# Kernel optimization log

Hardware: AMD Instinct MI355X
Metric: run time of the kernel (lower is better)

The kernel has to match this reference:

```python
import jax, jax.numpy as jnp
import numpy as np

LOWERSIZE = 40


def setup_inputs() -> dict:
    key = jax.random.key(0)
    ks = jax.random.split(key, 6)
    N, x_dim, y_dim = 2048, 768, 768
    return {
        "x_samples": jax.random.normal(ks[0], (N, x_dim), dtype=jnp.float32),
        "y_samples": jax.random.normal(ks[1], (N, y_dim), dtype=jnp.float32),
        "W1": jax.random.normal(ks[2], (LOWERSIZE, x_dim + y_dim), dtype=jnp.float32) * 0.02,
        "b1": jax.random.normal(ks[3], (LOWERSIZE,), dtype=jnp.float32) * 0.02,
        "W2": jax.random.normal(ks[4], (1, LOWERSIZE), dtype=jnp.float32) * 0.02,
        "b2": jax.random.normal(ks[5], (1,), dtype=jnp.float32) * 0.02,
    }


def reference(x_samples, y_samples, W1, b1, W2, b2):
    # F(z) = W2 @ relu(W1 @ z + b1) + b2, z = cat(x, y)
    N = y_samples.shape[0]
    x_dim = x_samples.shape[1]
    W1x = W1[:, :x_dim]   # [40, x_dim]
    W1y = W1[:, x_dim:]   # [40, y_dim]

    # Diagonal term T0: F(cat(x_i, y_i)) -> [N, 1]
    h0 = jax.nn.relu(x_samples @ W1x.T + y_samples @ W1y.T + b1)
    T0 = h0 @ W2.T + b2

    # Pairwise term: T1[i, j] = F(cat(x_j, y_i)) - 1.
    # Split the first Linear over x and y to avoid materializing the
    # [N, N, x_dim+y_dim] concatenation (same math, linearity of W1).
    hx = x_samples @ W1x.T  # [N, 40]
    hy = y_samples @ W1y.T  # [N, 40]
    h = jax.nn.relu(hy[:, None, :] + hx[None, :, :] + b1)  # [N, N, 40]
    T1 = (h @ W2.T + b2 - 1.0)[..., 0]  # [N, N]

    lse = jax.nn.logsumexp(T1, axis=1) - jnp.log(jnp.float32(N))  # [N]
    lower_bound = T0.mean() - jnp.exp(lse).mean()
    return lower_bound
```

## Files before the change

kernel.cpp:

```cpp
#include <hip/hip_runtime.h>

#define NROWS 2048
#define KDIM  768
#define L     40
#define KCH   6
#define KCSZ  128
#define HN    (NROWS * L)

__global__ __launch_bounds__(256) void k_proj(const float* __restrict__ x,
                                              const float* __restrict__ y,
                                              const float* __restrict__ W1,
                                              float* __restrict__ part) {
    const int kc    = blockIdx.y;
    const int which = blockIdx.z;
    const float* __restrict__ A = which ? y : x;
    const int tid = threadIdx.x;
    const int r   = tid >> 4;
    const int seg = tid & 15;
    const int row0 = blockIdx.x * 16;

    __shared__ float sh[16 * 688];

    const float* arow = A + (size_t)(row0 + r) * KDIM + kc * KCSZ;
    float4 a0 = *(const float4*)(arow + seg * 4);
    float4 a1 = *(const float4*)(arow + 64 + seg * 4);

    const float* wbase = W1 + (size_t)which * KDIM + kc * KCSZ;
#pragma unroll 8
    for (int o = 0; o < L; ++o) {
        const float* wrow = wbase + (size_t)o * (2 * KDIM);
        float4 w0 = *(const float4*)(wrow + seg * 4);
        float4 w1 = *(const float4*)(wrow + 64 + seg * 4);
        float s = a0.x * w0.x + a0.y * w0.y + a0.z * w0.z + a0.w * w0.w
                + a1.x * w1.x + a1.y * w1.y + a1.z * w1.z + a1.w * w1.w;
        sh[r * 688 + o * 17 + seg] = s;
    }
    __syncthreads();

    float* pout = part + (size_t)(kc * 2 + which) * HN + (size_t)row0 * L;
    for (int idx = tid; idx < 16 * L; idx += 256) {
        int rr = idx / L;
        int o  = idx - rr * L;
        float s = 0.f;
        int base = rr * 688 + o * 17;
#pragma unroll
        for (int q = 0; q < 16; ++q) s += sh[base + q];
        pout[idx] = s;
    }
}

__global__ __launch_bounds__(256) void k_red(const float* __restrict__ part,
                                             const float* __restrict__ b1,
                                             float* __restrict__ hxb,
                                             float* __restrict__ hy) {
    int gid = blockIdx.x * 256 + threadIdx.x;
    int which = gid / HN;
    int rem   = gid - which * HN;
    float s = 0.f;
#pragma unroll
    for (int kc = 0; kc < KCH; ++kc)
        s += part[(size_t)(kc * 2 + which) * HN + rem];
    if (!which) {
        s += b1[rem % L];
        hxb[rem] = s;
    } else {
        hy[rem] = s;
    }
}

#define BI 128
#define BJ 64
#define STRD 44

__global__ __launch_bounds__(512) void k_pair(const float* __restrict__ hxb,
                                              const float* __restrict__ hy,
                                              const float* __restrict__ W2,
                                              const float* __restrict__ b2p,
                                              float* __restrict__ pairE,
                                              float* __restrict__ pairT) {
    __shared__ float shy[BI * STRD];
    __shared__ float shx[BJ * STRD];
    __shared__ float sw2[STRD];
    __shared__ float red[16];

    const int tid = threadIdx.x;
    const int i0 = blockIdx.x * BI;
    const int j0 = blockIdx.y * BJ;

    for (int idx = tid; idx < BI * 10; idx += 512) {
        int rr = idx / 10, c = idx - rr * 10;
        float4 v = ((const float4*)(hy + (size_t)i0 * L))[idx];
        *(float4*)(shy + rr * STRD + c * 4) = v;
    }
    for (int idx = tid; idx < BJ * 10; idx += 512) {
        int rr = idx / 10, c = idx - rr * 10;
        float4 v = ((const float4*)(hxb + (size_t)j0 * L))[idx];
        *(float4*)(shx + rr * STRD + c * 4) = v;
    }
    if (tid < 10) ((float4*)sw2)[tid] = ((const float4*)W2)[tid];
    __syncthreads();

    const int tx = tid & 15, ty = tid >> 4;

    float acc[4][4];
#pragma unroll
    for (int u = 0; u < 4; ++u)
#pragma unroll
        for (int v = 0; v < 4; ++v) acc[u][v] = 0.f;

#pragma unroll
    for (int k4 = 0; k4 < 10; ++k4) {
        float4 w = *(const float4*)(sw2 + k4 * 4);
        float4 ay[4], ax[4];
#pragma unroll
        for (int u = 0; u < 4; ++u)
            ay[u] = *(const float4*)(shy + (ty + 32 * u) * STRD + k4 * 4);
#pragma unroll
        for (int v = 0; v < 4; ++v)
            ax[v] = *(const float4*)(shx + (tx + 16 * v) * STRD + k4 * 4);
#pragma unroll
        for (int u = 0; u < 4; ++u)
#pragma unroll
            for (int v = 0; v < 4; ++v) {
                float t;
                t = ay[u].x + ax[v].x; t = fmaxf(t, 0.f); acc[u][v] += t * w.x;
                t = ay[u].y + ax[v].y; t = fmaxf(t, 0.f); acc[u][v] += t * w.y;
                t = ay[u].z + ax[v].z; t = fmaxf(t, 0.f); acc[u][v] += t * w.z;
                t = ay[u].w + ax[v].w; t = fmaxf(t, 0.f); acc[u][v] += t * w.w;
            }
    }

    const float b2v = b2p[0];
    const float c1  = b2v - 1.f;
    float sumE = 0.f, sumT = 0.f;
#pragma unroll
    for (int u = 0; u < 4; ++u)
#pragma unroll
        for (int v = 0; v < 4; ++v) {
            int gi = i0 + ty + 32 * u;
            int gj = j0 + tx + 16 * v;
            float val = acc[u][v];
            if (gi == gj) sumT += val + b2v;
            sumE += __expf(val + c1);
        }

#pragma unroll
    for (int off = 32; off > 0; off >>= 1) {
        sumE += __shfl_down(sumE, off);
        sumT += __shfl_down(sumT, off);
    }
    int wid = tid >> 6;
    if ((tid & 63) == 0) { red[wid] = sumE; red[8 + wid] = sumT; }
    __syncthreads();
    if (tid == 0) {
        float e = 0.f, t = 0.f;
#pragma unroll
        for (int q = 0; q < 8; ++q) { e += red[q]; t += red[8 + q]; }
        int bid = blockIdx.y * gridDim.x + blockIdx.x;
        pairE[bid] = e;
        pairT[bid] = t;
    }
}

__global__ __launch_bounds__(512) void k_fin(const float* __restrict__ pairE,
                                             const float* __restrict__ pairT,
                                             float* __restrict__ out) {
    __shared__ float red[16];
    const int tid = threadIdx.x;
    float e = pairE[tid];
    float t = pairT[tid];
#pragma unroll
    for (int off = 32; off > 0; off >>= 1) {
        e += __shfl_down(e, off);
        t += __shfl_down(t, off);
    }
    int wid = tid >> 6;
    if ((tid & 63) == 0) { red[wid] = e; red[8 + wid] = t; }
    __syncthreads();
    if (tid == 0) {
        float se = 0.f, st = 0.f;
#pragma unroll
        for (int q = 0; q < 8; ++q) { se += red[q]; st += red[8 + q]; }
        const float invN = 1.0f / (float)NROWS;
        out[0] = st * invN - se * invN * invN;
    }
}

extern "C" void kernel_launch(void* const* d_in, const int* in_sizes, int n_in,
                              void* d_out, int out_size, void* d_ws, size_t ws_size,
                              hipStream_t stream) {
    const float* x  = (const float*)d_in[0];
    const float* y  = (const float*)d_in[1];
    const float* W1 = (const float*)d_in[2];
    const float* b1 = (const float*)d_in[3];
    const float* W2 = (const float*)d_in[4];
    const float* b2 = (const float*)d_in[5];
    float* out = (float*)d_out;

    float* wsf   = (float*)d_ws;
    float* hxb   = wsf;
    float* hy    = hxb + HN;
    float* part  = hy + HN;
    float* pairE = part + (size_t)KCH * 2 * HN;
    float* pairT = pairE + 512;

    k_proj<<<dim3(NROWS / 16, KCH, 2), 256, 0, stream>>>(x, y, W1, part);
    k_red<<<(2 * HN) / 256, 256, 0, stream>>>(part, b1, hxb, hy);
    k_pair<<<dim3(NROWS / BI, NROWS / BJ), 512, 0, stream>>>(hxb, hy, W2, b2, pairE, pairT);
    k_fin<<<1, 512, 0, stream>>>(pairE, pairT, out);
}
```

Before: 99.99 us.

## Process two rows per thread in projection and double-buffer pair kernel LDS loads

The projection kernel now has each thread handle two rows, so each W1 load is reused twice. It pre-reduces the partial sums with a cross-lane shuffle, which halves shared-memory stores and the final reduction work, and the grid shrinks accordingly. The pair kernel manually double-buffers its LDS operand loads across k4 steps and adds a min-blocks-per-CU launch bound so loads can overlap the ReLU/FMA work. The double buffering raises register pressure and could hurt occupancy despite the hint.

```diff
diff --git a/kernel.cpp b/kernel.cpp
--- a/kernel.cpp
+++ b/kernel.cpp
@@ -6,6 +6,8 @@
 #define KCH   6
 #define KCSZ  128
 #define HN    (NROWS * L)
+
+#define PSTR 328
 
 __global__ __launch_bounds__(256) void k_proj(const float* __restrict__ x,
                                               const float* __restrict__ y,
@@ -17,13 +19,16 @@
     const int tid = threadIdx.x;
     const int r   = tid >> 4;
     const int seg = tid & 15;
-    const int row0 = blockIdx.x * 16;
-
-    __shared__ float sh[16 * 688];
-
-    const float* arow = A + (size_t)(row0 + r) * KDIM + kc * KCSZ;
-    float4 a0 = *(const float4*)(arow + seg * 4);
-    float4 a1 = *(const float4*)(arow + 64 + seg * 4);
+    const int row0 = blockIdx.x * 32;
+
+    __shared__ float sh[32 * PSTR];
+
+    const float* arowA = A + (size_t)(row0 + r) * KDIM + kc * KCSZ;
+    const float* arowB = A + (size_t)(row0 + 16 + r) * KDIM + kc * KCSZ;
+    float4 a0 = *(const float4*)(arowA + seg * 4);
+    float4 a1 = *(const float4*)(arowA + 64 + seg * 4);
+    float4 b0 = *(const float4*)(arowB + seg * 4);
+    float4 b1 = *(const float4*)(arowB + 64 + seg * 4);
 
     const float* wbase = W1 + (size_t)which * KDIM + kc * KCSZ;
 #pragma unroll 8
@@ -31,21 +36,28 @@
         const float* wrow = wbase + (size_t)o * (2 * KDIM);
         float4 w0 = *(const float4*)(wrow + seg * 4);
         float4 w1 = *(const float4*)(wrow + 64 + seg * 4);
-        float s = a0.x * w0.x + a0.y * w0.y + a0.z * w0.z + a0.w * w0.w
-                + a1.x * w1.x + a1.y * w1.y + a1.z * w1.z + a1.w * w1.w;
-        sh[r * 688 + o * 17 + seg] = s;
+        float sA = a0.x * w0.x + a0.y * w0.y + a0.z * w0.z + a0.w * w0.w
+                 + a1.x * w1.x + a1.y * w1.y + a1.z * w1.z + a1.w * w1.w;
+        float sB = b0.x * w0.x + b0.y * w0.y + b0.z * w0.z + b0.w * w0.w
+                 + b1.x * w1.x + b1.y * w1.y + b1.z * w1.z + b1.w * w1.w;
+        sA += __shfl_xor(sA, 8);
+        sB += __shfl_xor(sB, 8);
+        if (seg < 8) {
+            sh[r * PSTR + o * 8 + seg] = sA;
+            sh[(r + 16) * PSTR + o * 8 + seg] = sB;
+        }
     }
     __syncthreads();
 
     float* pout = part + (size_t)(kc * 2 + which) * HN + (size_t)row0 * L;
-    for (int idx = tid; idx < 16 * L; idx += 256) {
+#pragma unroll
+    for (int k = 0; k < 5; ++k) {
+        int idx = tid + k * 256;
         int rr = idx / L;
         int o  = idx - rr * L;
-        float s = 0.f;
-        int base = rr * 688 + o * 17;
-#pragma unroll
-        for (int q = 0; q < 16; ++q) s += sh[base + q];
-        pout[idx] = s;
+        const float4* p = (const float4*)(sh + rr * PSTR + o * 8);
+        float4 u0 = p[0], u1 = p[1];
+        pout[idx] = u0.x + u0.y + u0.z + u0.w + u1.x + u1.y + u1.z + u1.w;
     }
 }
 
@@ -72,12 +84,12 @@
 #define BJ 64
 #define STRD 44
 
-__global__ __launch_bounds__(512) void k_pair(const float* __restrict__ hxb,
-                                              const float* __restrict__ hy,
-                                              const float* __restrict__ W2,
-                                              const float* __restrict__ b2p,
-                                              float* __restrict__ pairE,
-                                              float* __restrict__ pairT) {
+__global__ __launch_bounds__(512, 4) void k_pair(const float* __restrict__ hxb,
+                                                 const float* __restrict__ hy,
+                                                 const float* __restrict__ W2,
+                                                 const float* __restrict__ b2p,
+                                                 float* __restrict__ pairE,
+                                                 float* __restrict__ pairT) {
     __shared__ float shy[BI * STRD];
     __shared__ float shx[BJ * STRD];
     __shared__ float sw2[STRD];
@@ -108,27 +120,43 @@
 #pragma unroll
         for (int v = 0; v < 4; ++v) acc[u][v] = 0.f;
 
-#pragma unroll
-    for (int k4 = 0; k4 < 10; ++k4) {
-        float4 w = *(const float4*)(sw2 + k4 * 4);
-        float4 ay[4], ax[4];
-#pragma unroll
-        for (int u = 0; u < 4; ++u)
-            ay[u] = *(const float4*)(shy + (ty + 32 * u) * STRD + k4 * 4);
-#pragma unroll
-        for (int v = 0; v < 4; ++v)
-            ax[v] = *(const float4*)(shx + (tx + 16 * v) * STRD + k4 * 4);
-#pragma unroll
-        for (int u = 0; u < 4; ++u)
-#pragma unroll
-            for (int v = 0; v < 4; ++v) {
-                float t;
-                t = ay[u].x + ax[v].x; t = fmaxf(t, 0.f); acc[u][v] += t * w.x;
-                t = ay[u].y + ax[v].y; t = fmaxf(t, 0.f); acc[u][v] += t * w.y;
-                t = ay[u].z + ax[v].z; t = fmaxf(t, 0.f); acc[u][v] += t * w.z;
-                t = ay[u].w + ax[v].w; t = fmaxf(t, 0.f); acc[u][v] += t * w.w;
-            }
-    }
+    float4 ayA[4], axA[4], wA4;
+    float4 ayB[4], axB[4], wB4;
+
+#define LOADF(AY, AX, W4, K4) do {                                          \
+    W4 = *(const float4*)(sw2 + (K4) * 4);                                  \
+    _Pragma("unroll") for (int u_ = 0; u_ < 4; ++u_)                        \
+        AY[u_] = *(const float4*)(shy + (ty + 32 * u_) * STRD + (K4) * 4);  \
+    _Pragma("unroll") for (int v_ = 0; v_ < 4; ++v_)                        \
+        AX[v_] = *(const float4*)(shx + (tx + 16 * v_) * STRD + (K4) * 4);  \
+} while (0)
+
+#define FMAF(AY, AX, W4) do {                                               \
+    _Pragma("unroll") for (int u_ = 0; u_ < 4; ++u_)                        \
+    _Pragma("unroll") for (int v_ = 0; v_ < 4; ++v_) {                      \
+        float t;                                                            \
+        t = AY[u_].x + AX[v_].x; t = fmaxf(t, 0.f); acc[u_][v_] += t * W4.x;\
+        t = AY[u_].y + AX[v_].y; t = fmaxf(t, 0.f); acc[u_][v_] += t * W4.y;\
+        t = AY[u_].z + AX[v_].z; t = fmaxf(t, 0.f); acc[u_][v_] += t * W4.z;\
+        t = AY[u_].w + AX[v_].w; t = fmaxf(t, 0.f); acc[u_][v_] += t * W4.w;\
+    }                                                                       \
+} while (0)
+
+    LOADF(ayA, axA, wA4, 0);
+    LOADF(ayB, axB, wB4, 1);
+    FMAF(ayA, axA, wA4); LOADF(ayA, axA, wA4, 2);
+    FMAF(ayB, axB, wB4); LOADF(ayB, axB, wB4, 3);
+    FMAF(ayA, axA, wA4); LOADF(ayA, axA, wA4, 4);
+    FMAF(ayB, axB, wB4); LOADF(ayB, axB, wB4, 5);
+    FMAF(ayA, axA, wA4); LOADF(ayA, axA, wA4, 6);
+    FMAF(ayB, axB, wB4); LOADF(ayB, axB, wB4, 7);
+    FMAF(ayA, axA, wA4); LOADF(ayA, axA, wA4, 8);
+    FMAF(ayB, axB, wB4); LOADF(ayB, axB, wB4, 9);
+    FMAF(ayA, axA, wA4);
+    FMAF(ayB, axB, wB4);
+
+#undef LOADF
+#undef FMAF
 
     const float b2v = b2p[0];
     const float c1  = b2v - 1.f;
@@ -204,7 +232,7 @@
     float* pairE = part + (size_t)KCH * 2 * HN;
     float* pairT = pairE + 512;
 
-    k_proj<<<dim3(NROWS / 16, KCH, 2), 256, 0, stream>>>(x, y, W1, part);
+    k_proj<<<dim3(NROWS / 32, KCH, 2), 256, 0, stream>>>(x, y, W1, part);
     k_red<<<(2 * HN) / 256, 256, 0, stream>>>(part, b1, hxb, hy);
     k_pair<<<dim3(NROWS / BI, NROWS / BJ), 512, 0, stream>>>(hxb, hy, W2, b2, pairE, pairT);
     k_fin<<<1, 512, 0, stream>>>(pairE, pairT, out);
```

After: 101.0 us. About the same (+1.0%).
